# Performance work log

Hardware: AMD Instinct MI355X
Metric: run time of the kernel (lower is better)

Reference implementation:

```python
import jax, jax.numpy as jnp
import numpy as np

JITTER_NOISE = 0.01


def setup_inputs() -> dict:
    key = jax.random.key(0)
    k1, k2, k3 = jax.random.split(key, 3)
    B, S, H, E = 8, 4096, 2048, 64
    token_inputs = jax.random.normal(k1, (B, S, H), dtype=jnp.float32)
    # multiplicative jitter in [1 - eps, 1 + eps]
    jitter = jax.random.uniform(k2, (B, S, H), dtype=jnp.float32,
                                minval=1.0 - JITTER_NOISE, maxval=1.0 + JITTER_NOISE)
    w = jax.random.normal(k3, (H, E), dtype=jnp.float32) * 0.02
    b = jnp.zeros((E,), dtype=jnp.float32)
    return {"token_inputs": token_inputs, "jitter": jitter, "w": w, "b": b,
            "num_experts": E, "top_k": 2}


def reference(token_inputs, jitter, w, b, num_experts, top_k):
    # float32 routing computation with jitter noise
    x = token_inputs.astype(jnp.float32) * jitter
    # router logits: [B, S, E]
    logits = jnp.einsum('bsh,he->bse', x, w) + b
    probs = jax.nn.softmax(logits, axis=-1)  # [B, S, E]
    # top-k one-hot mask over experts
    top_k_indices = jax.lax.top_k(probs, top_k)[1]          # [B, S, K]
    mask = jax.nn.one_hot(top_k_indices, num_experts,
                          dtype=jnp.float32).sum(axis=-2)    # [B, S, E]
    return probs * mask
```

## Files before the change

### kernel.cpp

```cpp
#include <hip/hip_runtime.h>


#define H   2048
#define E   64
#define NKS 64

typedef __attribute__((ext_vector_type(8))) short bf16x8;
typedef __attribute__((ext_vector_type(4))) float f32x4;

__device__ inline ushort f2bf_rne(float f) {
    union { float f; unsigned u; } c; c.f = f;
    const unsigned r = (c.u + 0x7FFFu + ((c.u >> 16) & 1u)) >> 16;
    return (ushort)r;
}
__device__ inline float bf2f(ushort h) {
    union { unsigned u; float f; } c; c.u = ((unsigned)h) << 16;
    return c.f;
}

__global__ __launch_bounds__(256)
void wpack_kernel(const float* __restrict__ w, ushort* __restrict__ bp)
{
    const int t    = blockIdx.x * 256 + threadIdx.x;
    const int lane = t & 63;
    const int n    = (t >> 6) & 3;
    const int ks   = t >> 8;
    const int c    = lane & 15, g = lane >> 4;

    const float* src = w + (size_t)(ks * 32 + g * 8) * E + n * 16 + c;
    bf16x8 vh, vl;
#pragma unroll
    for (int s = 0; s < 8; ++s) {
        const float  v = src[(size_t)s * E];
        const ushort h = f2bf_rne(v);
        vh[s] = (short)h;
        vl[s] = (short)f2bf_rne(v - bf2f(h));
    }
    ushort* d = bp + ((size_t)(ks * 4 + n) * 2 * 64 + lane) * 8;
    *(bf16x8*)d         = vh;
    *(bf16x8*)(d + 512) = vl;
}

__global__ __launch_bounds__(256, 2)
void router_kernel(const float* __restrict__ xg,
                   const float* __restrict__ jg,
                   const ushort* __restrict__ bp,
                   const float* __restrict__ bias,
                   float* __restrict__ out)
{
    __shared__ __align__(16) float prod[4][2][16][8][4];

    const int tid  = threadIdx.x;
    const int wv   = tid >> 6;
    const int lane = tid & 63;
    const int ln   = lane & 15;
    const int g    = lane >> 4;
    const size_t tokBase = (size_t)blockIdx.x * 64 + (size_t)wv * 16;

    const int stok = lane >> 3;
    const int sf   = lane & 7;
    const int swf  = sf ^ (stok & 7);
    const float* xb = xg + (tokBase + stok) * H + sf * 4;
    const float* jb = jg + (tokBase + stok) * H + sf * 4;

    f32x4 acc[4];
#pragma unroll
    for (int n = 0; n < 4; ++n) acc[n] = (f32x4){0.f, 0.f, 0.f, 0.f};

    float4 xe0, xe1, je0, je1;
    float4 xo0, xo1, jo0, jo1;
    bf16x8 BH0[4], BL0[4], BH1[4], BL1[4];

#define LOAD_XJ(X0, J0, X1, J1, c) do {                         \
        const size_t o_ = (size_t)(c) * 32;                     \
        X0 = *(const float4*)(xb + o_);                         \
        J0 = *(const float4*)(jb + o_);                         \
        X1 = *(const float4*)(xb + o_ + 8 * (size_t)H);         \
        J1 = *(const float4*)(jb + o_ + 8 * (size_t)H);         \
    } while (0)

#define WRITE_STAGE(b, X0, J0, X1, J1) do {                     \
        float4 q0, q1;                                          \
        q0.x = X0.x * J0.x; q0.y = X0.y * J0.y;                 \
        q0.z = X0.z * J0.z; q0.w = X0.w * J0.w;                 \
        q1.x = X1.x * J1.x; q1.y = X1.y * J1.y;                 \
        q1.z = X1.z * J1.z; q1.w = X1.w * J1.w;                 \
        *(float4*)&prod[wv][b][stok][swf][0]     = q0;          \
        *(float4*)&prod[wv][b][stok + 8][swf][0] = q1;          \
    } while (0)

#define LOAD_B(BH, BL, ks) do {                                             \
        _Pragma("unroll")                                                   \
        for (int n_ = 0; n_ < 4; ++n_) {                                    \
            const ushort* p_ = bp + (size_t)((ks) * 4 + n_) * 1024 + lane * 8; \
            BH[n_] = *(const bf16x8*)p_;                                    \
            BL[n_] = *(const bf16x8*)(p_ + 512);                            \
        }                                                                   \
    } while (0)

#define KSTEP(rb, BH, BL) do {                                              \
        const int f0s_ = (g * 2) ^ (ln & 7);                                \
        float p_[8];                                                        \
        *(float4*)&p_[0] = *(const float4*)&prod[wv][rb][ln][f0s_][0];      \
        *(float4*)&p_[4] = *(const float4*)&prod[wv][rb][ln][f0s_ ^ 1][0];  \
        bf16x8 ah_, al_;                                                    \
        _Pragma("unroll")                                                   \
        for (int i_ = 0; i_ < 8; ++i_) {                                    \
            const ushort h_ = f2bf_rne(p_[i_]);                             \
            ah_[i_] = (short)h_;                                            \
            al_[i_] = (short)f2bf_rne(p_[i_] - bf2f(h_));                   \
        }                                                                   \
        _Pragma("unroll")                                                   \
        for (int n_ = 0; n_ < 4; ++n_) {                                    \
            acc[n_] = __builtin_amdgcn_mfma_f32_16x16x32_bf16(ah_, BH[n_], acc[n_], 0, 0, 0); \
            acc[n_] = __builtin_amdgcn_mfma_f32_16x16x32_bf16(al_, BH[n_], acc[n_], 0, 0, 0); \
            acc[n_] = __builtin_amdgcn_mfma_f32_16x16x32_bf16(ah_, BL[n_], acc[n_], 0, 0, 0); \
        }                                                                   \
    } while (0)

    LOAD_XJ(xe0, je0, xe1, je1, 0);
    LOAD_XJ(xo0, jo0, xo1, jo1, 1);
    LOAD_B(BH0, BL0, 0);
    WRITE_STAGE(0, xe0, je0, xe1, je1);

    for (int c = 0; c < NKS; c += 2) {
        {
            const int cl = (c + 2 < NKS) ? c + 2 : NKS - 1;
            LOAD_XJ(xe0, je0, xe1, je1, cl);
            const int kl = (c + 1 < NKS) ? c + 1 : NKS - 1;
            LOAD_B(BH1, BL1, kl);
            KSTEP(0, BH0, BL0);
            WRITE_STAGE(1, xo0, jo0, xo1, jo1);
        }
        {
            const int cl = (c + 3 < NKS) ? c + 3 : NKS - 1;
            LOAD_XJ(xo0, jo0, xo1, jo1, cl);
            const int kl = (c + 2 < NKS) ? c + 2 : NKS - 1;
            LOAD_B(BH0, BL0, kl);
            KSTEP(1, BH1, BL1);
            WRITE_STAGE(0, xe0, je0, xe1, je1);
        }
    }

    const float b0 = bias[ln], b1 = bias[16 + ln], b2 = bias[32 + ln], b3 = bias[48 + ln];
    float* outw = out + tokBase * E;

#pragma unroll
    for (int r = 0; r < 4; ++r) {
        const float v0 = acc[0][r] + b0;
        const float v1 = acc[1][r] + b1;
        const float v2 = acc[2][r] + b2;
        const float v3 = acc[3][r] + b3;

        float p1 = v0; int i1 = ln;
        float p2 = -3.0e38f; int i2 = ln;
        if (v1 > p1)      { p2 = p1; i2 = i1; p1 = v1; i1 = 16 + ln; }
        else if (v1 > p2) { p2 = v1; i2 = 16 + ln; }
        if (v2 > p1)      { p2 = p1; i2 = i1; p1 = v2; i1 = 32 + ln; }
        else if (v2 > p2) { p2 = v2; i2 = 32 + ln; }
        if (v3 > p1)      { p2 = p1; i2 = i1; p1 = v3; i1 = 48 + ln; }
        else if (v3 > p2) { p2 = v3; i2 = 48 + ln; }

#pragma unroll
        for (int m = 1; m <= 8; m <<= 1) {
            const float q1 = __shfl_xor(p1, m, 16);
            const int   k1 = __shfl_xor(i1, m, 16);
            const float q2 = __shfl_xor(p2, m, 16);
            const int   k2 = __shfl_xor(i2, m, 16);
            const bool  bw = (q1 > p1) || (q1 == p1 && k1 < i1);
            const float f1 = bw ? q1 : p1;  const int fi1 = bw ? k1 : i1;
            const float lo = bw ? p1 : q1;  const int loi = bw ? i1 : k1;
            const float sn = bw ? q2 : p2;  const int sni = bw ? k2 : i2;
            const bool  rw = (lo > sn) || (lo == sn && loi < sni);
            p2 = rw ? lo : sn;  i2 = rw ? loi : sni;
            p1 = f1;            i1 = fi1;
        }

        float d = __expf(v0 - p1) + __expf(v1 - p1) + __expf(v2 - p1) + __expf(v3 - p1);
#pragma unroll
        for (int m = 1; m <= 8; m <<= 1) d += __shfl_xor(d, m, 16);

        const float inv = 1.f / d;
        const float w2  = __expf(p2 - p1) * inv;

        const size_t trow = (size_t)(g * 4 + r) * E;
        outw[trow +      ln] = (     ln == i1) ? inv : (     ln == i2) ? w2 : 0.f;
        outw[trow + 16 + ln] = (16 + ln == i1) ? inv : (16 + ln == i2) ? w2 : 0.f;
        outw[trow + 32 + ln] = (32 + ln == i1) ? inv : (32 + ln == i2) ? w2 : 0.f;
        outw[trow + 48 + ln] = (48 + ln == i1) ? inv : (48 + ln == i2) ? w2 : 0.f;
    }
}

extern "C" void kernel_launch(void* const* d_in, const int* in_sizes, int n_in,
                              void* d_out, int out_size, void* d_ws, size_t ws_size,
                              hipStream_t stream)
{
    const float* x   = (const float*)d_in[0];
    const float* jit = (const float*)d_in[1];
    const float* w   = (const float*)d_in[2];
    const float* b   = (const float*)d_in[3];
    float*       out = (float*)d_out;

    ushort* bpack = (ushort*)d_ws;

    hipLaunchKernelGGL(wpack_kernel, dim3(64), dim3(256), 0, stream, w, bpack);

    const int n_tok = in_sizes[0] / H;
    dim3 grid(n_tok / 64), block(256);
    hipLaunchKernelGGL(router_kernel, grid, block, 0, stream,
                       x, jit, bpack, b, out);
}
```

Measured before the change: 122.5 us.

## Split K across wave pairs and stage bf16 hi/lo splits in LDS

Each block now covers 32 tokens, and its four waves split the hidden dimension in two halves: waves 2-3 compute the upper K half and pass partial accumulators through LDS to waves 0-1, which finish the softmax and top-2. The fp32-to-bf16 hi/lo split now happens once when data is written to LDS instead of after reading it, and only one B register set is kept, which together with launch bounds raised to 4 blocks should lower register use and raise occupancy. The grid doubles, which gives more parallelism on a memory-bound stream over x and jitter. The costs are an extra syncthreads and reduction, idle waves during the epilogue, and B loads that are no longer prefetched ahead of the MFMAs.

Result: slower. 147.8 us (+20.7%).

```diff
diff --git a/kernel.cpp b/kernel.cpp
--- a/kernel.cpp
+++ b/kernel.cpp
@@ -1,9 +1,9 @@
 #include <hip/hip_runtime.h>
 
 
-#define H   2048
-#define E   64
-#define NKS 64
+#define H    2048
+#define E    64
+#define NKS2 32
 
 typedef __attribute__((ext_vector_type(8))) short bf16x8;
 typedef __attribute__((ext_vector_type(4))) float f32x4;
@@ -41,106 +41,114 @@
     *(bf16x8*)(d + 512) = vl;
 }
 
-__global__ __launch_bounds__(256, 2)
+__global__ __launch_bounds__(256, 4)
 void router_kernel(const float* __restrict__ xg,
                    const float* __restrict__ jg,
                    const ushort* __restrict__ bp,
                    const float* __restrict__ bias,
                    float* __restrict__ out)
 {
-    __shared__ __align__(16) float prod[4][2][16][8][4];
+    __shared__ ushort stg[4][2][2][16][32];
+    __shared__ float  red[2][64][20];
 
     const int tid  = threadIdx.x;
     const int wv   = tid >> 6;
     const int lane = tid & 63;
     const int ln   = lane & 15;
     const int g    = lane >> 4;
-    const size_t tokBase = (size_t)blockIdx.x * 64 + (size_t)wv * 16;
-
-    const int stok = lane >> 3;
-    const int sf   = lane & 7;
-    const int swf  = sf ^ (stok & 7);
-    const float* xb = xg + (tokBase + stok) * H + sf * 4;
-    const float* jb = jg + (tokBase + stok) * H + sf * 4;
+    const int wtok = (wv & 1) << 4;
+    const int kh   = wv >> 1;
+    const size_t tokBase = (size_t)blockIdx.x * 32 + wtok;
+
+    const int stok = lane >> 2;
+    const int sk8  = (lane & 3) << 3;
+    const float* xb = xg + (tokBase + stok) * H + kh * 1024 + sk8;
+    const float* jb = jg + (tokBase + stok) * H + kh * 1024 + sk8;
+    const ushort* bpw = bp + (size_t)kh * 131072 + (size_t)lane * 8;
 
     f32x4 acc[4];
 #pragma unroll
     for (int n = 0; n < 4; ++n) acc[n] = (f32x4){0.f, 0.f, 0.f, 0.f};
 
-    float4 xe0, xe1, je0, je1;
+    float4 xa0, xa1, ja0, ja1;
     float4 xo0, xo1, jo0, jo1;
-    bf16x8 BH0[4], BL0[4], BH1[4], BL1[4];
-
-#define LOAD_XJ(X0, J0, X1, J1, c) do {                         \
-        const size_t o_ = (size_t)(c) * 32;                     \
-        X0 = *(const float4*)(xb + o_);                         \
-        J0 = *(const float4*)(jb + o_);                         \
-        X1 = *(const float4*)(xb + o_ + 8 * (size_t)H);         \
-        J1 = *(const float4*)(jb + o_ + 8 * (size_t)H);         \
-    } while (0)
-
-#define WRITE_STAGE(b, X0, J0, X1, J1) do {                     \
-        float4 q0, q1;                                          \
-        q0.x = X0.x * J0.x; q0.y = X0.y * J0.y;                 \
-        q0.z = X0.z * J0.z; q0.w = X0.w * J0.w;                 \
-        q1.x = X1.x * J1.x; q1.y = X1.y * J1.y;                 \
-        q1.z = X1.z * J1.z; q1.w = X1.w * J1.w;                 \
-        *(float4*)&prod[wv][b][stok][swf][0]     = q0;          \
-        *(float4*)&prod[wv][b][stok + 8][swf][0] = q1;          \
-    } while (0)
-
-#define LOAD_B(BH, BL, ks) do {                                             \
-        _Pragma("unroll")                                                   \
-        for (int n_ = 0; n_ < 4; ++n_) {                                    \
-            const ushort* p_ = bp + (size_t)((ks) * 4 + n_) * 1024 + lane * 8; \
-            BH[n_] = *(const bf16x8*)p_;                                    \
-            BL[n_] = *(const bf16x8*)(p_ + 512);                            \
-        }                                                                   \
-    } while (0)
-
-#define KSTEP(rb, BH, BL) do {                                              \
-        const int f0s_ = (g * 2) ^ (ln & 7);                                \
-        float p_[8];                                                        \
-        *(float4*)&p_[0] = *(const float4*)&prod[wv][rb][ln][f0s_][0];      \
-        *(float4*)&p_[4] = *(const float4*)&prod[wv][rb][ln][f0s_ ^ 1][0];  \
-        bf16x8 ah_, al_;                                                    \
-        _Pragma("unroll")                                                   \
-        for (int i_ = 0; i_ < 8; ++i_) {                                    \
-            const ushort h_ = f2bf_rne(p_[i_]);                             \
-            ah_[i_] = (short)h_;                                            \
-            al_[i_] = (short)f2bf_rne(p_[i_] - bf2f(h_));                   \
-        }                                                                   \
-        _Pragma("unroll")                                                   \
-        for (int n_ = 0; n_ < 4; ++n_) {                                    \
+    bf16x8 BH[4], BL[4];
+
+#define LOAD_XJ(X0, X1, J0, J1, c) do {                 \
+        const size_t o_ = (size_t)(c) * 32;             \
+        X0 = *(const float4*)(xb + o_);                 \
+        X1 = *(const float4*)(xb + o_ + 4);             \
+        J0 = *(const float4*)(jb + o_);                 \
+        J1 = *(const float4*)(jb + o_ + 4);             \
+    } while (0)
+
+#define STAGEW(b, X0, X1, J0, J1) do {                  \
+        float p_[8];                                    \
+        p_[0] = X0.x * J0.x; p_[1] = X0.y * J0.y;       \
+        p_[2] = X0.z * J0.z; p_[3] = X0.w * J0.w;       \
+        p_[4] = X1.x * J1.x; p_[5] = X1.y * J1.y;       \
+        p_[6] = X1.z * J1.z; p_[7] = X1.w * J1.w;       \
+        bf16x8 vh_, vl_;                                \
+        _Pragma("unroll")                               \
+        for (int i_ = 0; i_ < 8; ++i_) {                \
+            const ushort h_ = f2bf_rne(p_[i_]);         \
+            vh_[i_] = (short)h_;                        \
+            vl_[i_] = (short)f2bf_rne(p_[i_] - bf2f(h_)); \
+        }                                               \
+        *(bf16x8*)&stg[wv][b][0][stok][sk8] = vh_;      \
+        *(bf16x8*)&stg[wv][b][1][stok][sk8] = vl_;      \
+    } while (0)
+
+#define LOAD_B(c) do {                                              \
+        _Pragma("unroll")                                           \
+        for (int n_ = 0; n_ < 4; ++n_) {                            \
+            const ushort* p_ = bpw + (size_t)((c) * 4 + n_) * 1024; \
+            BH[n_] = *(const bf16x8*)p_;                            \
+            BL[n_] = *(const bf16x8*)(p_ + 512);                    \
+        }                                                           \
+    } while (0)
+
+#define KSTEP(b) do {                                               \
+        const bf16x8 ah_ = *(const bf16x8*)&stg[wv][b][0][ln][g * 8]; \
+        const bf16x8 al_ = *(const bf16x8*)&stg[wv][b][1][ln][g * 8]; \
+        _Pragma("unroll")                                           \
+        for (int n_ = 0; n_ < 4; ++n_) {                            \
             acc[n_] = __builtin_amdgcn_mfma_f32_16x16x32_bf16(ah_, BH[n_], acc[n_], 0, 0, 0); \
             acc[n_] = __builtin_amdgcn_mfma_f32_16x16x32_bf16(al_, BH[n_], acc[n_], 0, 0, 0); \
             acc[n_] = __builtin_amdgcn_mfma_f32_16x16x32_bf16(ah_, BL[n_], acc[n_], 0, 0, 0); \
-        }                                                                   \
-    } while (0)
-
-    LOAD_XJ(xe0, je0, xe1, je1, 0);
-    LOAD_XJ(xo0, jo0, xo1, jo1, 1);
-    LOAD_B(BH0, BL0, 0);
-    WRITE_STAGE(0, xe0, je0, xe1, je1);
-
-    for (int c = 0; c < NKS; c += 2) {
-        {
-            const int cl = (c + 2 < NKS) ? c + 2 : NKS - 1;
-            LOAD_XJ(xe0, je0, xe1, je1, cl);
-            const int kl = (c + 1 < NKS) ? c + 1 : NKS - 1;
-            LOAD_B(BH1, BL1, kl);
-            KSTEP(0, BH0, BL0);
-            WRITE_STAGE(1, xo0, jo0, xo1, jo1);
-        }
-        {
-            const int cl = (c + 3 < NKS) ? c + 3 : NKS - 1;
-            LOAD_XJ(xo0, jo0, xo1, jo1, cl);
-            const int kl = (c + 2 < NKS) ? c + 2 : NKS - 1;
-            LOAD_B(BH0, BL0, kl);
-            KSTEP(1, BH1, BL1);
-            WRITE_STAGE(0, xe0, je0, xe1, je1);
-        }
-    }
+        }                                                           \
+    } while (0)
+
+    LOAD_XJ(xa0, xa1, ja0, ja1, 0);
+    LOAD_XJ(xo0, xo1, jo0, jo1, 1);
+    STAGEW(0, xa0, xa1, ja0, ja1);
+
+#pragma unroll 1
+    for (int c = 0; c < NKS2; c += 2) {
+        if (c + 2 < NKS2) LOAD_XJ(xa0, xa1, ja0, ja1, c + 2);
+        __builtin_amdgcn_sched_barrier(0);
+        if (c + 1 < NKS2) STAGEW(1, xo0, xo1, jo0, jo1);
+        LOAD_B(c);
+        KSTEP(0);
+        if (c + 3 < NKS2) LOAD_XJ(xo0, xo1, jo0, jo1, c + 3);
+        __builtin_amdgcn_sched_barrier(0);
+        if (c + 2 < NKS2) STAGEW(0, xa0, xa1, ja0, ja1);
+        LOAD_B(c + 1);
+        KSTEP(1);
+    }
+
+    if (kh == 1) {
+        const int w2 = wv - 2;
+#pragma unroll
+        for (int n = 0; n < 4; ++n)
+            *(f32x4*)&red[w2][lane][n << 2] = acc[n];
+    }
+    __syncthreads();
+    if (kh == 1) return;
+
+#pragma unroll
+    for (int n = 0; n < 4; ++n)
+        acc[n] += *(const f32x4*)&red[wv][lane][n << 2];
 
     const float b0 = bias[ln], b1 = bias[16 + ln], b2 = bias[32 + ln], b3 = bias[48 + ln];
     float* outw = out + tokBase * E;
@@ -181,13 +189,13 @@
         for (int m = 1; m <= 8; m <<= 1) d += __shfl_xor(d, m, 16);
 
         const float inv = 1.f / d;
-        const float w2  = __expf(p2 - p1) * inv;
+        const float w2p = __expf(p2 - p1) * inv;
 
         const size_t trow = (size_t)(g * 4 + r) * E;
-        outw[trow +      ln] = (     ln == i1) ? inv : (     ln == i2) ? w2 : 0.f;
-        outw[trow + 16 + ln] = (16 + ln == i1) ? inv : (16 + ln == i2) ? w2 : 0.f;
-        outw[trow + 32 + ln] = (32 + ln == i1) ? inv : (32 + ln == i2) ? w2 : 0.f;
-        outw[trow + 48 + ln] = (48 + ln == i1) ? inv : (48 + ln == i2) ? w2 : 0.f;
+        outw[trow +      ln] = (     ln == i1) ? inv : (     ln == i2) ? w2p : 0.f;
+        outw[trow + 16 + ln] = (16 + ln == i1) ? inv : (16 + ln == i2) ? w2p : 0.f;
+        outw[trow + 32 + ln] = (32 + ln == i1) ? inv : (32 + ln == i2) ? w2p : 0.f;
+        outw[trow + 48 + ln] = (48 + ln == i1) ? inv : (48 + ln == i2) ? w2p : 0.f;
     }
 }
 
@@ -206,7 +214,7 @@
     hipLaunchKernelGGL(wpack_kernel, dim3(64), dim3(256), 0, stream, w, bpack);
 
     const int n_tok = in_sizes[0] / H;
-    dim3 grid(n_tok / 64), block(256);
+    dim3 grid(n_tok / 32), block(256);
     hipLaunchKernelGGL(router_kernel, grid, block, 0, stream,
                        x, jit, bpack, b, out);
 }
```

## Stage x, jitter and packed weights via direct global-to-LDS loads with 2x2 wave tiling

Applied to the files above, without the earlier changes.

The router kernel now moves x, jitter and the packed bf16 weight tiles straight into shared memory with global_load_lds, double-buffered and separated by block barriers. The register prefetch path and per-wave B-register loads go away. Each block now handles 32 tokens split across waves as 2 token halves by 2 expert halves, and the launch bound asks for 4 blocks per CU instead of 2. The softmax and top-2 epilogue now goes through an LDS logits tile so each thread can write one token's outputs as coalesced float4 stores. The cost is a __syncthreads per K step and more LDS per block.

After: 135.5 us. 10.6% more time.

```diff
diff --git a/kernel.cpp b/kernel.cpp
--- a/kernel.cpp
+++ b/kernel.cpp
@@ -7,6 +7,9 @@
 
 typedef __attribute__((ext_vector_type(8))) short bf16x8;
 typedef __attribute__((ext_vector_type(4))) float f32x4;
+
+#define GBL(p)  ((const __attribute__((address_space(1))) void*)(p))
+#define LDSP(p) ((__attribute__((address_space(3))) void*)(p))
 
 __device__ inline ushort f2bf_rne(float f) {
     union { float f; unsigned u; } c; c.f = f;
@@ -41,154 +44,158 @@
     *(bf16x8*)(d + 512) = vl;
 }
 
-__global__ __launch_bounds__(256, 2)
+__global__ __launch_bounds__(256, 4)
 void router_kernel(const float* __restrict__ xg,
                    const float* __restrict__ jg,
                    const ushort* __restrict__ bp,
                    const float* __restrict__ bias,
                    float* __restrict__ out)
 {
-    __shared__ __align__(16) float prod[4][2][16][8][4];
+    __shared__ __align__(16) unsigned char smem[32768];
+    float  (*xs)[32][32] = (float (*)[32][32])(void*)smem;
+    float  (*js)[32][32] = (float (*)[32][32])(void*)(smem + 8192);
+    ushort (*bs)[512]    = (ushort (*)[512])(void*)(smem + 16384);
 
     const int tid  = threadIdx.x;
     const int wv   = tid >> 6;
     const int lane = tid & 63;
     const int ln   = lane & 15;
     const int g    = lane >> 4;
-    const size_t tokBase = (size_t)blockIdx.x * 64 + (size_t)wv * 16;
-
-    const int stok = lane >> 3;
-    const int sf   = lane & 7;
-    const int swf  = sf ^ (stok & 7);
-    const float* xb = xg + (tokBase + stok) * H + sf * 4;
-    const float* jb = jg + (tokBase + stok) * H + sf * 4;
-
-    f32x4 acc[4];
-#pragma unroll
-    for (int n = 0; n < 4; ++n) acc[n] = (f32x4){0.f, 0.f, 0.f, 0.f};
-
-    float4 xe0, xe1, je0, je1;
-    float4 xo0, xo1, jo0, jo1;
-    bf16x8 BH0[4], BL0[4], BH1[4], BL1[4];
-
-#define LOAD_XJ(X0, J0, X1, J1, c) do {                         \
-        const size_t o_ = (size_t)(c) * 32;                     \
-        X0 = *(const float4*)(xb + o_);                         \
-        J0 = *(const float4*)(jb + o_);                         \
-        X1 = *(const float4*)(xb + o_ + 8 * (size_t)H);         \
-        J1 = *(const float4*)(jb + o_ + 8 * (size_t)H);         \
+    const int mh   = wv >> 1;
+    const int nh   = wv & 1;
+    const size_t tokBase = (size_t)blockIdx.x * 32;
+
+    const int srow = lane >> 3;
+    const int sqd  = ((lane & 7) - srow) & 7;
+    const float* xsb = xg + (tokBase + wv * 8 + srow) * (size_t)H + sqd * 4;
+    const float* jsb = jg + (tokBase + wv * 8 + srow) * (size_t)H + sqd * 4;
+    const ushort* bsb = bp + (size_t)wv * 1024 + (size_t)lane * 8;
+
+    const int t = mh * 16 + ln;
+
+    f32x4 acc0 = (f32x4){0.f, 0.f, 0.f, 0.f};
+    f32x4 acc1 = (f32x4){0.f, 0.f, 0.f, 0.f};
+
+#define STAGE(b, c) do {                                                      \
+        __builtin_amdgcn_global_load_lds(GBL(xsb + (size_t)(c) * 32),         \
+                                         LDSP(&xs[b][wv * 8][0]), 16, 0, 0);  \
+        __builtin_amdgcn_global_load_lds(GBL(jsb + (size_t)(c) * 32),         \
+                                         LDSP(&js[b][wv * 8][0]), 16, 0, 0);  \
+        __builtin_amdgcn_global_load_lds(GBL(bsb + (size_t)(c) * 4096),       \
+                                         LDSP(&bs[(b) * 8 + wv * 2][0]), 16, 0, 0); \
+        __builtin_amdgcn_global_load_lds(GBL(bsb + (size_t)(c) * 4096 + 512), \
+                                         LDSP(&bs[(b) * 8 + wv * 2 + 1][0]), 16, 0, 0); \
     } while (0)
 
-#define WRITE_STAGE(b, X0, J0, X1, J1) do {                     \
-        float4 q0, q1;                                          \
-        q0.x = X0.x * J0.x; q0.y = X0.y * J0.y;                 \
-        q0.z = X0.z * J0.z; q0.w = X0.w * J0.w;                 \
-        q1.x = X1.x * J1.x; q1.y = X1.y * J1.y;                 \
-        q1.z = X1.z * J1.z; q1.w = X1.w * J1.w;                 \
-        *(float4*)&prod[wv][b][stok][swf][0]     = q0;          \
-        *(float4*)&prod[wv][b][stok + 8][swf][0] = q1;          \
+#define COMPUTE(b) do {                                                       \
+        const int p0 = ((2 * g + t) & 7) << 2;                                \
+        const int p1 = ((2 * g + 1 + t) & 7) << 2;                            \
+        const float4 xq0 = *(const float4*)&xs[b][t][p0];                     \
+        const float4 xq1 = *(const float4*)&xs[b][t][p1];                     \
+        const float4 jq0 = *(const float4*)&js[b][t][p0];                     \
+        const float4 jq1 = *(const float4*)&js[b][t][p1];                     \
+        float pr[8];                                                          \
+        pr[0] = xq0.x * jq0.x; pr[1] = xq0.y * jq0.y;                         \
+        pr[2] = xq0.z * jq0.z; pr[3] = xq0.w * jq0.w;                         \
+        pr[4] = xq1.x * jq1.x; pr[5] = xq1.y * jq1.y;                         \
+        pr[6] = xq1.z * jq1.z; pr[7] = xq1.w * jq1.w;                         \
+        bf16x8 ah, al;                                                        \
+        _Pragma("unroll")                                                     \
+        for (int i_ = 0; i_ < 8; ++i_) {                                      \
+            const ushort h_ = f2bf_rne(pr[i_]);                               \
+            ah[i_] = (short)h_;                                               \
+            al[i_] = (short)f2bf_rne(pr[i_] - bf2f(h_));                      \
+        }                                                                     \
+        const bf16x8 BH0 = *(const bf16x8*)&bs[(b) * 8 + 4 * nh + 0][lane * 8]; \
+        const bf16x8 BL0 = *(const bf16x8*)&bs[(b) * 8 + 4 * nh + 1][lane * 8]; \
+        const bf16x8 BH1 = *(const bf16x8*)&bs[(b) * 8 + 4 * nh + 2][lane * 8]; \
+        const bf16x8 BL1 = *(const bf16x8*)&bs[(b) * 8 + 4 * nh + 3][lane * 8]; \
+        acc0 = __builtin_amdgcn_mfma_f32_16x16x32_bf16(ah, BH0, acc0, 0, 0, 0); \
+        acc0 = __builtin_amdgcn_mfma_f32_16x16x32_bf16(al, BH0, acc0, 0, 0, 0); \
+        acc0 = __builtin_amdgcn_mfma_f32_16x16x32_bf16(ah, BL0, acc0, 0, 0, 0); \
+        acc1 = __builtin_amdgcn_mfma_f32_16x16x32_bf16(ah, BH1, acc1, 0, 0, 0); \
+        acc1 = __builtin_amdgcn_mfma_f32_16x16x32_bf16(al, BH1, acc1, 0, 0, 0); \
+        acc1 = __builtin_amdgcn_mfma_f32_16x16x32_bf16(ah, BL1, acc1, 0, 0, 0); \
     } while (0)
 
-#define LOAD_B(BH, BL, ks) do {                                             \
-        _Pragma("unroll")                                                   \
-        for (int n_ = 0; n_ < 4; ++n_) {                                    \
-            const ushort* p_ = bp + (size_t)((ks) * 4 + n_) * 1024 + lane * 8; \
-            BH[n_] = *(const bf16x8*)p_;                                    \
-            BL[n_] = *(const bf16x8*)(p_ + 512);                            \
-        }                                                                   \
-    } while (0)
-
-#define KSTEP(rb, BH, BL) do {                                              \
-        const int f0s_ = (g * 2) ^ (ln & 7);                                \
-        float p_[8];                                                        \
-        *(float4*)&p_[0] = *(const float4*)&prod[wv][rb][ln][f0s_][0];      \
-        *(float4*)&p_[4] = *(const float4*)&prod[wv][rb][ln][f0s_ ^ 1][0];  \
-        bf16x8 ah_, al_;                                                    \
-        _Pragma("unroll")                                                   \
-        for (int i_ = 0; i_ < 8; ++i_) {                                    \
-            const ushort h_ = f2bf_rne(p_[i_]);                             \
-            ah_[i_] = (short)h_;                                            \
-            al_[i_] = (short)f2bf_rne(p_[i_] - bf2f(h_));                   \
-        }                                                                   \
-        _Pragma("unroll")                                                   \
-        for (int n_ = 0; n_ < 4; ++n_) {                                    \
-            acc[n_] = __builtin_amdgcn_mfma_f32_16x16x32_bf16(ah_, BH[n_], acc[n_], 0, 0, 0); \
-            acc[n_] = __builtin_amdgcn_mfma_f32_16x16x32_bf16(al_, BH[n_], acc[n_], 0, 0, 0); \
-            acc[n_] = __builtin_amdgcn_mfma_f32_16x16x32_bf16(ah_, BL[n_], acc[n_], 0, 0, 0); \
-        }                                                                   \
-    } while (0)
-
-    LOAD_XJ(xe0, je0, xe1, je1, 0);
-    LOAD_XJ(xo0, jo0, xo1, jo1, 1);
-    LOAD_B(BH0, BL0, 0);
-    WRITE_STAGE(0, xe0, je0, xe1, je1);
-
+    STAGE(0, 0);
+    __syncthreads();
+
+#pragma unroll 1
     for (int c = 0; c < NKS; c += 2) {
-        {
-            const int cl = (c + 2 < NKS) ? c + 2 : NKS - 1;
-            LOAD_XJ(xe0, je0, xe1, je1, cl);
-            const int kl = (c + 1 < NKS) ? c + 1 : NKS - 1;
-            LOAD_B(BH1, BL1, kl);
-            KSTEP(0, BH0, BL0);
-            WRITE_STAGE(1, xo0, jo0, xo1, jo1);
-        }
-        {
-            const int cl = (c + 3 < NKS) ? c + 3 : NKS - 1;
-            LOAD_XJ(xo0, jo0, xo1, jo1, cl);
-            const int kl = (c + 2 < NKS) ? c + 2 : NKS - 1;
-            LOAD_B(BH0, BL0, kl);
-            KSTEP(1, BH1, BL1);
-            WRITE_STAGE(0, xe0, je0, xe1, je1);
-        }
-    }
-
-    const float b0 = bias[ln], b1 = bias[16 + ln], b2 = bias[32 + ln], b3 = bias[48 + ln];
-    float* outw = out + tokBase * E;
-
+        STAGE(1, c + 1);
+        __builtin_amdgcn_sched_barrier(0);
+        COMPUTE(0);
+        __syncthreads();
+        if (c + 2 < NKS) STAGE(0, c + 2);
+        __builtin_amdgcn_sched_barrier(0);
+        COMPUTE(1);
+        __syncthreads();
+    }
+
+    float (*lgx)[68] = (float (*)[68])(void*)smem;
 #pragma unroll
     for (int r = 0; r < 4; ++r) {
-        const float v0 = acc[0][r] + b0;
-        const float v1 = acc[1][r] + b1;
-        const float v2 = acc[2][r] + b2;
-        const float v3 = acc[3][r] + b3;
-
-        float p1 = v0; int i1 = ln;
-        float p2 = -3.0e38f; int i2 = ln;
-        if (v1 > p1)      { p2 = p1; i2 = i1; p1 = v1; i1 = 16 + ln; }
-        else if (v1 > p2) { p2 = v1; i2 = 16 + ln; }
-        if (v2 > p1)      { p2 = p1; i2 = i1; p1 = v2; i1 = 32 + ln; }
-        else if (v2 > p2) { p2 = v2; i2 = 32 + ln; }
-        if (v3 > p1)      { p2 = p1; i2 = i1; p1 = v3; i1 = 48 + ln; }
-        else if (v3 > p2) { p2 = v3; i2 = 48 + ln; }
-
-#pragma unroll
-        for (int m = 1; m <= 8; m <<= 1) {
-            const float q1 = __shfl_xor(p1, m, 16);
-            const int   k1 = __shfl_xor(i1, m, 16);
-            const float q2 = __shfl_xor(p2, m, 16);
-            const int   k2 = __shfl_xor(i2, m, 16);
-            const bool  bw = (q1 > p1) || (q1 == p1 && k1 < i1);
-            const float f1 = bw ? q1 : p1;  const int fi1 = bw ? k1 : i1;
-            const float lo = bw ? p1 : q1;  const int loi = bw ? i1 : k1;
-            const float sn = bw ? q2 : p2;  const int sni = bw ? k2 : i2;
-            const bool  rw = (lo > sn) || (lo == sn && loi < sni);
-            p2 = rw ? lo : sn;  i2 = rw ? loi : sni;
-            p1 = f1;            i1 = fi1;
-        }
-
-        float d = __expf(v0 - p1) + __expf(v1 - p1) + __expf(v2 - p1) + __expf(v3 - p1);
-#pragma unroll
-        for (int m = 1; m <= 8; m <<= 1) d += __shfl_xor(d, m, 16);
-
-        const float inv = 1.f / d;
-        const float w2  = __expf(p2 - p1) * inv;
-
-        const size_t trow = (size_t)(g * 4 + r) * E;
-        outw[trow +      ln] = (     ln == i1) ? inv : (     ln == i2) ? w2 : 0.f;
-        outw[trow + 16 + ln] = (16 + ln == i1) ? inv : (16 + ln == i2) ? w2 : 0.f;
-        outw[trow + 32 + ln] = (32 + ln == i1) ? inv : (32 + ln == i2) ? w2 : 0.f;
-        outw[trow + 48 + ln] = (48 + ln == i1) ? inv : (48 + ln == i2) ? w2 : 0.f;
-    }
+        lgx[mh * 16 + g * 4 + r][nh * 32 + ln]      = acc0[r];
+        lgx[mh * 16 + g * 4 + r][nh * 32 + 16 + ln] = acc1[r];
+    }
+    __syncthreads();
+
+    const int t8 = tid >> 3;
+    const int q8 = tid & 7;
+    float l[8];
+    *(float4*)&l[0] = *(const float4*)&lgx[t8][q8 * 8];
+    *(float4*)&l[4] = *(const float4*)&lgx[t8][q8 * 8 + 4];
+    const float4 bb0 = *(const float4*)(bias + q8 * 8);
+    const float4 bb1 = *(const float4*)(bias + q8 * 8 + 4);
+    l[0] += bb0.x; l[1] += bb0.y; l[2] += bb0.z; l[3] += bb0.w;
+    l[4] += bb1.x; l[5] += bb1.y; l[6] += bb1.z; l[7] += bb1.w;
+
+    float p1 = l[0]; int i1 = q8 * 8;
+    float p2 = -3.0e38f; int i2 = q8 * 8;
+#pragma unroll
+    for (int i = 1; i < 8; ++i) {
+        const int e = q8 * 8 + i;
+        if (l[i] > p1)      { p2 = p1; i2 = i1; p1 = l[i]; i1 = e; }
+        else if (l[i] > p2) { p2 = l[i]; i2 = e; }
+    }
+
+#pragma unroll
+    for (int m = 1; m <= 4; m <<= 1) {
+        const float q1 = __shfl_xor(p1, m, 8);
+        const int   k1 = __shfl_xor(i1, m, 8);
+        const float q2 = __shfl_xor(p2, m, 8);
+        const int   k2 = __shfl_xor(i2, m, 8);
+        const bool  bw = (q1 > p1) || (q1 == p1 && k1 < i1);
+        const float f1 = bw ? q1 : p1;  const int fi1 = bw ? k1 : i1;
+        const float lo = bw ? p1 : q1;  const int loi = bw ? i1 : k1;
+        const float sn = bw ? q2 : p2;  const int sni = bw ? k2 : i2;
+        const bool  rw = (lo > sn) || (lo == sn && loi < sni);
+        p2 = rw ? lo : sn;  i2 = rw ? loi : sni;
+        p1 = f1;            i1 = fi1;
+    }
+
+    float d = 0.f;
+#pragma unroll
+    for (int i = 0; i < 8; ++i) d += __expf(l[i] - p1);
+#pragma unroll
+    for (int m = 1; m <= 4; m <<= 1) d += __shfl_xor(d, m, 8);
+
+    const float inv = 1.f / d;
+    const float w2  = __expf(p2 - p1) * inv;
+
+    float* op = out + (tokBase + t8) * (size_t)E + q8 * 8;
+    float4 v0, v1;
+    v0.x = (q8 * 8 + 0 == i1) ? inv : (q8 * 8 + 0 == i2) ? w2 : 0.f;
+    v0.y = (q8 * 8 + 1 == i1) ? inv : (q8 * 8 + 1 == i2) ? w2 : 0.f;
+    v0.z = (q8 * 8 + 2 == i1) ? inv : (q8 * 8 + 2 == i2) ? w2 : 0.f;
+    v0.w = (q8 * 8 + 3 == i1) ? inv : (q8 * 8 + 3 == i2) ? w2 : 0.f;
+    v1.x = (q8 * 8 + 4 == i1) ? inv : (q8 * 8 + 4 == i2) ? w2 : 0.f;
+    v1.y = (q8 * 8 + 5 == i1) ? inv : (q8 * 8 + 5 == i2) ? w2 : 0.f;
+    v1.z = (q8 * 8 + 6 == i1) ? inv : (q8 * 8 + 6 == i2) ? w2 : 0.f;
+    v1.w = (q8 * 8 + 7 == i1) ? inv : (q8 * 8 + 7 == i2) ? w2 : 0.f;
+    *(float4*)op       = v0;
+    *(float4*)(op + 4) = v1;
 }
 
 extern "C" void kernel_launch(void* const* d_in, const int* in_sizes, int n_in,
@@ -206,7 +213,7 @@
     hipLaunchKernelGGL(wpack_kernel, dim3(64), dim3(256), 0, stream, w, bpack);
 
     const int n_tok = in_sizes[0] / H;
-    dim3 grid(n_tok / 64), block(256);
+    dim3 grid(n_tok / 32), block(256);
     hipLaunchKernelGGL(router_kernel, grid, block, 0, stream,
                        x, jit, bpack, b, out);
 }
```
